# Kernel optimization log

Measured on AMD Instinct MI355X. Metric: run time of the kernel, lower is better.

The kernel has to match this reference:

```python
import jax, jax.numpy as jnp
import numpy as np

COUNTS = (16, 8, 8)  # num_scale_layers from __init__


def _conv1d(x, w, b):
    # x: [B, C, L], w: [Cout, Cin, K] (torch Conv1d layout), valid padding, stride 1
    y = jax.lax.conv_general_dilated(
        x, w, window_strides=(1,), padding='VALID',
        dimension_numbers=('NCH', 'OIH', 'NCH'))
    return y + b[None, :, None]


def _maxpool3s2(x):
    # MaxPool1d(kernel=3, stride=2), valid padding
    return jax.lax.reduce_window(x, -jnp.inf, jax.lax.max,
                                 (1, 1, 3), (1, 1, 2), 'VALID')


def setup_inputs() -> dict:
    key = jax.random.key(0)
    ks = jax.random.split(key, 5)
    B, C, N = 64, 512, 64
    scale = 0.03  # ~1/sqrt(C*K), keeps deep relu-conv chain numerically sane
    x = jax.random.normal(ks[0], (B, C, N), jnp.float32)
    w1 = jax.random.normal(ks[1], (C, C, 1), jnp.float32) * scale
    b1 = jax.random.normal(ks[2], (C,), jnp.float32) * scale
    n_k2 = sum(COUNTS) - len(COUNTS)  # 29 kernel-size-2 convs
    w2 = jax.random.normal(ks[3], (n_k2, C, C, 2), jnp.float32) * scale
    b2 = jax.random.normal(ks[4], (n_k2, C), jnp.float32) * scale
    return {"x": x, "w1": w1, "b1": b1, "w2": w2, "b2": b2}


def reference(x, w1, b1, w2, b2):
    B, C, N = x.shape
    x2d = jnp.zeros((B, C, N, N), x.dtype)
    mask = np.eye(N, dtype=bool)  # static: indices are compile-time constants
    k2 = 0
    stride, offset = 1, 0
    for level, count in enumerate(COUNTS):
        for order in range(count):
            if level == 0 and order == 0:
                x = jax.nn.relu(_conv1d(x, w1, b1))
            elif level > 0 and order == 0:
                x = jax.nn.relu(_maxpool3s2(x))
            else:
                x = jax.nn.relu(_conv1d(x, w2[k2], b2[k2]))
                k2 += 1
            i = np.arange(0, N - offset, stride)
            j = np.arange(offset, N, stride)
            # scatter conv output onto strided diagonal of the 2D map
            x2d = x2d.at[:, :, i, j].set(x)
            mask[i, j] = True
            offset += stride
        offset += stride
        stride *= 2
    return x2d, jnp.asarray(mask)
```

## Files before the change

kernel.cpp:

```cpp
#include <hip/hip_runtime.h>

typedef _Float16 f16;
typedef f16 f16x8 __attribute__((ext_vector_type(8)));
typedef f16 f16x4 __attribute__((ext_vector_type(4)));
typedef float f32x4 __attribute__((ext_vector_type(4)));

#define B_ 64
#define C_ 512
#define X2D_ELEMS ((size_t)134217728)
#define CHAIN_PITCH 1104

__device__ __forceinline__ int col_of(int i, int j) {
    const int d = j - i;
    if (d < 0) return -1;
    if (d <= 15) return 64 * d - (d * (d - 1)) / 2 + i;
    if (d >= 17 && d <= 31 && (d & 1) && !(i & 1)) {
        const int v = (d - 17) >> 1;
        return 904 + 24 * v - (v * (v - 1)) / 2 + (i >> 1);
    }
    if (d >= 35 && !((d - 35) & 3) && !(i & 3)) {
        const int v = (d - 35) >> 2;
        return 1068 + 8 * v - (v * (v - 1)) / 2 + (i >> 2);
    }
    return -1;
}

template<int K, int TAPS>
__device__ __forceinline__
void conv_body(const f16* S, const f16* __restrict__ Wl,
               const float* __restrict__ bias, f16* __restrict__ chain,
               int b0, int q, int cb_out, int Lin, int Lout, int G)
{
    const int lane = threadIdx.x & 63, w = threadIdx.x >> 6;
    const int colq = lane & 15, kg = lane >> 4;
    const int cobase = q * 128 + w * 32;
    const f16* wp0 = Wl + (size_t)(cobase + colq) * K + (kg << 3);
    const f16* wp1 = wp0 + (size_t)16 * K;

    int vg[4], vl[4], row0[4]; bool val[4];
    #pragma unroll
    for (int nf = 0; nf < 4; nf++) {
        const int v = nf * 16 + colq;
        vg[nf] = v / Lout; vl[nf] = v - vg[nf] * Lout;
        val[nf] = vg[nf] < G;
        row0[nf] = val[nf] ? vg[nf] * Lin + vl[nf] : 0;
    }

    f32x4 acc0[4] = {}, acc1[4] = {};
    #pragma unroll 4
    for (int k0 = 0; k0 < K; k0 += 32) {
        const f16x8 af0 = *(const f16x8*)(wp0 + k0);
        const f16x8 af1 = *(const f16x8*)(wp1 + k0);
        const int t = (TAPS == 2 && k0 >= 512) ? 1 : 0;
        const int cch = ((k0 & 511) >> 3) + kg;
        #pragma unroll
        for (int nf = 0; nf < 4; nf++) {
            const int r = row0[nf] + t;
            const f16x8 bf = *(const f16x8*)&S[(r << 9) + ((cch ^ (r & 7)) << 3)];
            acc0[nf] = __builtin_amdgcn_mfma_f32_16x16x32_f16(af0, bf, acc0[nf], 0, 0, 0);
            acc1[nf] = __builtin_amdgcn_mfma_f32_16x16x32_f16(af1, bf, acc1[nf], 0, 0, 0);
        }
    }

    const int co0 = cobase + (kg << 2);
    const float4 bb0 = *(const float4*)&bias[co0];
    const float4 bb1 = *(const float4*)&bias[co0 + 16];
    #pragma unroll
    for (int nf = 0; nf < 4; nf++) {
        if (!val[nf]) continue;
        const size_t base = (((size_t)(b0 + vg[nf]) * CHAIN_PITCH + cb_out + vl[nf]) << 9);
        f16x4 h0, h1;
        #pragma unroll
        for (int j = 0; j < 4; j++) {
            h0[j] = (f16)fmaxf(acc0[nf][j] + ((const float*)&bb0)[j], 0.0f);
            h1[j] = (f16)fmaxf(acc1[nf][j] + ((const float*)&bb1)[j], 0.0f);
        }
        *(f16x4*)&chain[base + co0] = h0;
        *(f16x4*)&chain[base + co0 + 16] = h1;
    }
}

template<int POOL>
__global__ __launch_bounds__(256, 2)
void conv_k2(const f16* __restrict__ chainr, int cb_in,
             const f16* __restrict__ Wl, const float* __restrict__ bias,
             f16* __restrict__ chain, int cb_pool, int cb_out,
             int Lin, int Lout, int G)
{
    __shared__ __align__(16) f16 S[64 * 512];
    const int lane = threadIdx.x & 63, wv = threadIdx.x >> 6;
    const int b0 = blockIdx.x * G, q = blockIdx.y;
    const int rows = G * Lin;

    for (int r = wv; r < rows; r += 4) {
        const int g = r / Lin, l = r - g * Lin;
        f16x8 o;
        if (POOL) {
            const f16* src = chainr +
                (((size_t)(b0 + g) * CHAIN_PITCH + cb_in + 2 * l) << 9) + (lane << 3);
            const f16x8 s0 = *(const f16x8*)(src);
            const f16x8 s1 = *(const f16x8*)(src + 512);
            const f16x8 s2 = *(const f16x8*)(src + 1024);
            #pragma unroll
            for (int j = 0; j < 8; j++)
                o[j] = (f16)fmaxf(fmaxf((float)s0[j], (float)s1[j]),
                                  fmaxf((float)s2[j], 0.0f));
            if (q == 0)
                *(f16x8*)&chain[(((size_t)(b0 + g) * CHAIN_PITCH + cb_pool + l) << 9)
                                + (lane << 3)] = o;
        } else {
            o = *(const f16x8*)(chainr +
                (((size_t)(b0 + g) * CHAIN_PITCH + cb_in + l) << 9) + (lane << 3));
        }
        *(f16x8*)&S[(r << 9) + ((lane ^ (r & 7)) << 3)] = o;
    }
    __syncthreads();
    conv_body<1024, 2>(S, Wl, bias, chain, b0, q, cb_out, Lin, Lout, G);
}

__global__ __launch_bounds__(256, 2)
void conv_first(const float* __restrict__ x, const f16* __restrict__ Wf,
                const float* __restrict__ b1, f16* __restrict__ chain)
{
    __shared__ __align__(16) f16 S[64 * 512];
    const int tid = threadIdx.x;
    const int b = blockIdx.x, q = blockIdx.y;
    #pragma unroll 4
    for (int p = 0; p < 32; p++) {
        const int ci = p * 16 + (tid >> 4), l0 = (tid & 15) << 2;
        const float4 v = *(const float4*)&x[(((size_t)b * C_ + ci) << 6) + l0];
        #pragma unroll
        for (int j = 0; j < 4; j++) {
            const int r = l0 + j;
            S[(r << 9) + (((ci >> 3) ^ (r & 7)) << 3) + (ci & 7)] =
                (f16)((const float*)&v)[j];
        }
    }
    __syncthreads();
    conv_body<512, 1>(S, Wf, b1, chain, b, q, 0, 64, 64, 1);
}

__global__ void prep_all(const float* __restrict__ w1, const float* __restrict__ w2,
                         f16* __restrict__ Wf, float* __restrict__ maskp)
{
    const unsigned idx = blockIdx.x * 256 + threadIdx.x;
    if (idx < 4096u)
        maskp[idx] = (col_of(idx >> 6, idx & 63) >= 0) ? 1.0f : 0.0f;
    if (idx < 262144u) {
        Wf[idx] = (f16)w1[idx];
    } else if (idx < 30u * 262144u) {
        const unsigned r = idx - 262144u;
        const int k2 = r >> 18;
        const unsigned rem = r & 262143u;
        const int co = rem >> 9, ci = rem & 511;
        const float2 v = *(const float2*)&w2[((((size_t)k2 << 9) + co) << 10) + (ci << 1)];
        f16* base = Wf + 262144 + ((size_t)k2 << 19) + ((size_t)co << 10);
        base[ci] = (f16)v.x;
        base[512 + ci] = (f16)v.y;
    }
}

__global__ __launch_bounds__(256)
void assemble3(const f16* __restrict__ chain, float* __restrict__ x2d)
{
    __shared__ __align__(16) f16 J[64 * 512];
    const int tid = threadIdx.x, lane = tid & 63, wv = tid >> 6;
    const int i = blockIdx.x, b = blockIdx.y;

    for (int j = wv; j < 64; j += 4) {
        const int col = col_of(i, j);
        f16x8 v = {0, 0, 0, 0, 0, 0, 0, 0};
        if (col >= 0)
            v = *(const f16x8*)(chain + (((size_t)b * CHAIN_PITCH + col) << 9) + (lane << 3));
        *(f16x8*)&J[(j << 9) + ((lane ^ (j & 7)) << 3)] = v;
    }
    __syncthreads();

    const int jq = tid & 15, c0 = tid >> 4;
    float* dst0 = x2d + (((size_t)b * C_) << 12) + (i << 6) + (jq << 2);
    for (int ct = 0; ct < 32; ct++) {
        const int c = c0 + (ct << 4);
        const int cj = c >> 3;
        float4 o;
        #pragma unroll
        for (int jj = 0; jj < 4; jj++) {
            const int j = (jq << 2) + jj;
            ((float*)&o)[jj] = (float)J[(j << 9) + ((cj ^ (j & 7)) << 3) + (c & 7)];
        }
        *(float4*)(dst0 + ((size_t)c << 12)) = o;
    }
}

extern "C" void kernel_launch(void* const* d_in, const int* in_sizes, int n_in,
                              void* d_out, int out_size, void* d_ws, size_t ws_size,
                              hipStream_t stream)
{
    const float* x  = (const float*)d_in[0];
    const float* w1 = (const float*)d_in[1];
    const float* b1 = (const float*)d_in[2];
    const float* w2 = (const float*)d_in[3];
    const float* b2 = (const float*)d_in[4];
    float* x2d   = (float*)d_out;
    float* maskp = x2d + X2D_ELEMS;

    f16* chain = (f16*)d_ws;
    f16* Wf    = (f16*)x2d;

    prep_all<<<(30 * 262144) / 256, 256, 0, stream>>>(w1, w2, Wf, maskp);

    conv_first<<<dim3(64, 4), 256, 0, stream>>>(x, Wf, b1, chain);

    int L = 64, cb = 64, prev = 0, k2 = 0;
    for (int i = 0; i < 15; i++) {
        conv_k2<0><<<dim3(64, 4), 256, 0, stream>>>(
            chain, prev, Wf + 262144 + (size_t)k2 * 524288, b2 + (size_t)k2 * C_,
            chain, 0, cb, L, L - 1, 1);
        k2++; prev = cb; cb += L - 1; L--;
    }

    conv_k2<1><<<dim3(32, 4), 256, 0, stream>>>(
        chain, prev, Wf + 262144 + (size_t)k2 * 524288, b2 + (size_t)k2 * C_,
        chain, 904, 928, 24, 23, 2);
    k2++; L = 23; prev = 928; cb = 951;
    for (int i = 0; i < 6; i++) {
        conv_k2<0><<<dim3(32, 4), 256, 0, stream>>>(
            chain, prev, Wf + 262144 + (size_t)k2 * 524288, b2 + (size_t)k2 * C_,
            chain, 0, cb, L, L - 1, 2);
        k2++; prev = cb; cb += L - 1; L--;
    }

    conv_k2<1><<<dim3(8, 4), 256, 0, stream>>>(
        chain, prev, Wf + 262144 + (size_t)k2 * 524288, b2 + (size_t)k2 * C_,
        chain, 1068, 1076, 8, 7, 8);
    k2++; L = 7; prev = 1076; cb = 1083;
    for (int i = 0; i < 6; i++) {
        conv_k2<0><<<dim3(8, 4), 256, 0, stream>>>(
            chain, prev, Wf + 262144 + (size_t)k2 * 524288, b2 + (size_t)k2 * C_,
            chain, 0, cb, L, L - 1, 8);
        k2++; prev = cb; cb += L - 1; L--;
    }

    assemble3<<<dim3(64, B_), 256, 0, stream>>>(chain, x2d);
}
```

Before: 759.4 us.

## Retile conv blocks to 64 output channels and overlap assembly with later convs

The conv kernels now tile 64 output channels by 64 positions per block, with a 2x2 wave arrangement, instead of 128 channels by all positions. That raises the block count from 256 to 512 for the early layers. The small-batch conv launches in levels 1 and 2 gain extra blocks that scatter already-finished rows of the 2D output map (rows of later-completed diagonals for batches 4 to 63) while the convs run. This is meant to fill idle CUs during the underoccupied tail layers. The final assembly kernel then only handles the remaining rows, which adds complexity to the indexing and to the ordering dependencies between chain columns.

```diff
diff --git a/kernel.cpp b/kernel.cpp
--- a/kernel.cpp
+++ b/kernel.cpp
@@ -27,76 +27,112 @@
 
 template<int K, int TAPS>
 __device__ __forceinline__
-void conv_body(const f16* S, const f16* __restrict__ Wl,
-               const float* __restrict__ bias, f16* __restrict__ chain,
-               int b0, int q, int cb_out, int Lin, int Lout, int G)
-{
-    const int lane = threadIdx.x & 63, w = threadIdx.x >> 6;
+void conv_body22(const f16* S, const f16* __restrict__ Wl,
+                 const float* __restrict__ bias, f16* __restrict__ chain,
+                 int b0, int m0, int cb_out, int Lin, int Lout, int G)
+{
+    const int lane = threadIdx.x & 63, wv = threadIdx.x >> 6;
+    const int wm = wv >> 1, wn = wv & 1;
     const int colq = lane & 15, kg = lane >> 4;
-    const int cobase = q * 128 + w * 32;
-    const f16* wp0 = Wl + (size_t)(cobase + colq) * K + (kg << 3);
+    const f16* wp0 = Wl + (size_t)(m0 + wm * 32 + colq) * K + (kg << 3);
     const f16* wp1 = wp0 + (size_t)16 * K;
 
-    int vg[4], vl[4], row0[4]; bool val[4];
+    int row0[2], vg[2], vl[2]; bool val[2];
     #pragma unroll
-    for (int nf = 0; nf < 4; nf++) {
-        const int v = nf * 16 + colq;
+    for (int nf = 0; nf < 2; nf++) {
+        const int v = wn * 32 + nf * 16 + colq;
         vg[nf] = v / Lout; vl[nf] = v - vg[nf] * Lout;
         val[nf] = vg[nf] < G;
         row0[nf] = val[nf] ? vg[nf] * Lin + vl[nf] : 0;
     }
 
-    f32x4 acc0[4] = {}, acc1[4] = {};
+    f32x4 acc00 = {}, acc01 = {}, acc10 = {}, acc11 = {};
     #pragma unroll 4
     for (int k0 = 0; k0 < K; k0 += 32) {
         const f16x8 af0 = *(const f16x8*)(wp0 + k0);
         const f16x8 af1 = *(const f16x8*)(wp1 + k0);
         const int t = (TAPS == 2 && k0 >= 512) ? 1 : 0;
         const int cch = ((k0 & 511) >> 3) + kg;
-        #pragma unroll
-        for (int nf = 0; nf < 4; nf++) {
-            const int r = row0[nf] + t;
-            const f16x8 bf = *(const f16x8*)&S[(r << 9) + ((cch ^ (r & 7)) << 3)];
-            acc0[nf] = __builtin_amdgcn_mfma_f32_16x16x32_f16(af0, bf, acc0[nf], 0, 0, 0);
-            acc1[nf] = __builtin_amdgcn_mfma_f32_16x16x32_f16(af1, bf, acc1[nf], 0, 0, 0);
-        }
-    }
-
-    const int co0 = cobase + (kg << 2);
+        const int r0 = row0[0] + t, r1 = row0[1] + t;
+        const f16x8 bf0 = *(const f16x8*)&S[(r0 << 9) + ((cch ^ (r0 & 7)) << 3)];
+        const f16x8 bf1 = *(const f16x8*)&S[(r1 << 9) + ((cch ^ (r1 & 7)) << 3)];
+        acc00 = __builtin_amdgcn_mfma_f32_16x16x32_f16(af0, bf0, acc00, 0, 0, 0);
+        acc10 = __builtin_amdgcn_mfma_f32_16x16x32_f16(af1, bf0, acc10, 0, 0, 0);
+        acc01 = __builtin_amdgcn_mfma_f32_16x16x32_f16(af0, bf1, acc01, 0, 0, 0);
+        acc11 = __builtin_amdgcn_mfma_f32_16x16x32_f16(af1, bf1, acc11, 0, 0, 0);
+    }
+
+    const int co0 = m0 + wm * 32 + (kg << 2);
     const float4 bb0 = *(const float4*)&bias[co0];
     const float4 bb1 = *(const float4*)&bias[co0 + 16];
     #pragma unroll
-    for (int nf = 0; nf < 4; nf++) {
+    for (int nf = 0; nf < 2; nf++) {
         if (!val[nf]) continue;
         const size_t base = (((size_t)(b0 + vg[nf]) * CHAIN_PITCH + cb_out + vl[nf]) << 9);
+        const f32x4 a0 = nf ? acc01 : acc00;
+        const f32x4 a1 = nf ? acc11 : acc10;
         f16x4 h0, h1;
         #pragma unroll
         for (int j = 0; j < 4; j++) {
-            h0[j] = (f16)fmaxf(acc0[nf][j] + ((const float*)&bb0)[j], 0.0f);
-            h1[j] = (f16)fmaxf(acc1[nf][j] + ((const float*)&bb1)[j], 0.0f);
+            h0[j] = (f16)fmaxf(a0[j] + ((const float*)&bb0)[j], 0.0f);
+            h1[j] = (f16)fmaxf(a1[j] + ((const float*)&bb1)[j], 0.0f);
         }
         *(f16x4*)&chain[base + co0] = h0;
         *(f16x4*)&chain[base + co0 + 16] = h1;
     }
 }
 
+__device__ __forceinline__
+void assemble_unit(f16* S, const f16* __restrict__ chain,
+                   float* __restrict__ x2d, int i, int b)
+{
+    const int tid = threadIdx.x, lane = tid & 63, wv = tid >> 6;
+    for (int j = wv; j < 64; j += 4) {
+        const int col = col_of(i, j);
+        f16x8 v = {0, 0, 0, 0, 0, 0, 0, 0};
+        if (col >= 0)
+            v = *(const f16x8*)(chain + (((size_t)b * CHAIN_PITCH + col) << 9) + (lane << 3));
+        *(f16x8*)&S[(j << 9) + ((lane ^ (j & 7)) << 3)] = v;
+    }
+    __syncthreads();
+    const int jq = tid & 15, c0 = tid >> 4;
+    float* dst0 = x2d + (((size_t)b * C_) << 12) + (i << 6) + (jq << 2);
+    for (int ct = 0; ct < 32; ct++) {
+        const int c = c0 + (ct << 4);
+        const int cj = c >> 3;
+        float4 o;
+        #pragma unroll
+        for (int jj = 0; jj < 4; jj++) {
+            const int j = (jq << 2) + jj;
+            ((float*)&o)[jj] = (float)S[(j << 9) + ((cj ^ (j & 7)) << 3) + (c & 7)];
+        }
+        *(float4*)(dst0 + ((size_t)c << 12)) = o;
+    }
+}
+
 template<int POOL>
 __global__ __launch_bounds__(256, 2)
-void conv_k2(const f16* __restrict__ chainr, int cb_in,
-             const f16* __restrict__ Wl, const float* __restrict__ bias,
-             f16* __restrict__ chain, int cb_pool, int cb_out,
-             int Lin, int Lout, int G)
+void conv_k2(int cb_in, const f16* __restrict__ Wl,
+             const float* __restrict__ bias, f16* __restrict__ chain,
+             int cb_pool, int cb_out, int Lin, int Lout, int G, int nbg,
+             float* __restrict__ x2d, int au_base, int au_tot, int row_base)
 {
     __shared__ __align__(16) f16 S[64 * 512];
+    if ((int)blockIdx.y >= nbg) {
+        const int u = au_base + ((int)blockIdx.y - nbg) * 8 + (int)blockIdx.x;
+        if (u >= au_tot) return;
+        assemble_unit(S, chain, x2d, row_base + u / 60, 4 + u % 60);
+        return;
+    }
     const int lane = threadIdx.x & 63, wv = threadIdx.x >> 6;
-    const int b0 = blockIdx.x * G, q = blockIdx.y;
+    const int b0 = blockIdx.y * G, m0 = blockIdx.x * 64;
     const int rows = G * Lin;
 
     for (int r = wv; r < rows; r += 4) {
         const int g = r / Lin, l = r - g * Lin;
         f16x8 o;
         if (POOL) {
-            const f16* src = chainr +
+            const f16* src = chain +
                 (((size_t)(b0 + g) * CHAIN_PITCH + cb_in + 2 * l) << 9) + (lane << 3);
             const f16x8 s0 = *(const f16x8*)(src);
             const f16x8 s1 = *(const f16x8*)(src + 512);
@@ -105,17 +141,17 @@
             for (int j = 0; j < 8; j++)
                 o[j] = (f16)fmaxf(fmaxf((float)s0[j], (float)s1[j]),
                                   fmaxf((float)s2[j], 0.0f));
-            if (q == 0)
+            if (blockIdx.x == 0)
                 *(f16x8*)&chain[(((size_t)(b0 + g) * CHAIN_PITCH + cb_pool + l) << 9)
                                 + (lane << 3)] = o;
         } else {
-            o = *(const f16x8*)(chainr +
+            o = *(const f16x8*)(chain +
                 (((size_t)(b0 + g) * CHAIN_PITCH + cb_in + l) << 9) + (lane << 3));
         }
         *(f16x8*)&S[(r << 9) + ((lane ^ (r & 7)) << 3)] = o;
     }
     __syncthreads();
-    conv_body<1024, 2>(S, Wl, bias, chain, b0, q, cb_out, Lin, Lout, G);
+    conv_body22<1024, 2>(S, Wl, bias, chain, b0, m0, cb_out, Lin, Lout, G);
 }
 
 __global__ __launch_bounds__(256, 2)
@@ -124,7 +160,7 @@
 {
     __shared__ __align__(16) f16 S[64 * 512];
     const int tid = threadIdx.x;
-    const int b = blockIdx.x, q = blockIdx.y;
+    const int b = blockIdx.y, m0 = blockIdx.x * 64;
     #pragma unroll 4
     for (int p = 0; p < 32; p++) {
         const int ci = p * 16 + (tid >> 4), l0 = (tid & 15) << 2;
@@ -137,7 +173,7 @@
         }
     }
     __syncthreads();
-    conv_body<512, 1>(S, Wf, b1, chain, b, q, 0, 64, 64, 1);
+    conv_body22<512, 1>(S, Wf, b1, chain, b, m0, 0, 64, 64, 1);
 }
 
 __global__ void prep_all(const float* __restrict__ w1, const float* __restrict__ w2,
@@ -161,34 +197,14 @@
 }
 
 __global__ __launch_bounds__(256)
-void assemble3(const f16* __restrict__ chain, float* __restrict__ x2d)
-{
-    __shared__ __align__(16) f16 J[64 * 512];
-    const int tid = threadIdx.x, lane = tid & 63, wv = tid >> 6;
-    const int i = blockIdx.x, b = blockIdx.y;
-
-    for (int j = wv; j < 64; j += 4) {
-        const int col = col_of(i, j);
-        f16x8 v = {0, 0, 0, 0, 0, 0, 0, 0};
-        if (col >= 0)
-            v = *(const f16x8*)(chain + (((size_t)b * CHAIN_PITCH + col) << 9) + (lane << 3));
-        *(f16x8*)&J[(j << 9) + ((lane ^ (j & 7)) << 3)] = v;
-    }
-    __syncthreads();
-
-    const int jq = tid & 15, c0 = tid >> 4;
-    float* dst0 = x2d + (((size_t)b * C_) << 12) + (i << 6) + (jq << 2);
-    for (int ct = 0; ct < 32; ct++) {
-        const int c = c0 + (ct << 4);
-        const int cj = c >> 3;
-        float4 o;
-        #pragma unroll
-        for (int jj = 0; jj < 4; jj++) {
-            const int j = (jq << 2) + jj;
-            ((float*)&o)[jj] = (float)J[(j << 9) + ((cj ^ (j & 7)) << 3) + (c & 7)];
-        }
-        *(float4*)(dst0 + ((size_t)c << 12)) = o;
-    }
+void assemble_fin(const f16* __restrict__ chain, float* __restrict__ x2d)
+{
+    __shared__ __align__(16) f16 S[64 * 512];
+    const int u = blockIdx.x;
+    int i, b;
+    if (u < 2112) { i = u >> 6; b = u & 63; }
+    else { const int v = u - 2112; i = 33 + (v >> 2); b = v & 3; }
+    assemble_unit(S, chain, x2d, i, b);
 }
 
 extern "C" void kernel_launch(void* const* d_in, const int* in_sizes, int n_in,
@@ -208,37 +224,37 @@
 
     prep_all<<<(30 * 262144) / 256, 256, 0, stream>>>(w1, w2, Wf, maskp);
 
-    conv_first<<<dim3(64, 4), 256, 0, stream>>>(x, Wf, b1, chain);
+    conv_first<<<dim3(8, 64), 256, 0, stream>>>(x, Wf, b1, chain);
 
     int L = 64, cb = 64, prev = 0, k2 = 0;
     for (int i = 0; i < 15; i++) {
-        conv_k2<0><<<dim3(64, 4), 256, 0, stream>>>(
-            chain, prev, Wf + 262144 + (size_t)k2 * 524288, b2 + (size_t)k2 * C_,
-            chain, 0, cb, L, L - 1, 1);
+        conv_k2<0><<<dim3(8, 64), 256, 0, stream>>>(
+            prev, Wf + 262144 + (size_t)k2 * 524288, b2 + (size_t)k2 * C_,
+            chain, 0, cb, L, L - 1, 1, 64, x2d, 0, 0, 0);
         k2++; prev = cb; cb += L - 1; L--;
     }
 
-    conv_k2<1><<<dim3(32, 4), 256, 0, stream>>>(
-        chain, prev, Wf + 262144 + (size_t)k2 * 524288, b2 + (size_t)k2 * C_,
-        chain, 904, 928, 24, 23, 2);
+    conv_k2<1><<<dim3(8, 52), 256, 0, stream>>>(
+        prev, Wf + 262144 + (size_t)k2 * 524288, b2 + (size_t)k2 * C_,
+        chain, 904, 928, 24, 23, 2, 32, x2d, 0, 1020, 47);
     k2++; L = 23; prev = 928; cb = 951;
     for (int i = 0; i < 6; i++) {
-        conv_k2<0><<<dim3(32, 4), 256, 0, stream>>>(
-            chain, prev, Wf + 262144 + (size_t)k2 * 524288, b2 + (size_t)k2 * C_,
-            chain, 0, cb, L, L - 1, 2);
+        conv_k2<0><<<dim3(8, 52), 256, 0, stream>>>(
+            prev, Wf + 262144 + (size_t)k2 * 524288, b2 + (size_t)k2 * C_,
+            chain, 0, cb, L, L - 1, 2, 32, x2d, (i + 1) * 160, 1020, 47);
         k2++; prev = cb; cb += L - 1; L--;
     }
 
-    conv_k2<1><<<dim3(8, 4), 256, 0, stream>>>(
-        chain, prev, Wf + 262144 + (size_t)k2 * 524288, b2 + (size_t)k2 * C_,
-        chain, 1068, 1076, 8, 7, 8);
+    conv_k2<1><<<dim3(8, 24), 256, 0, stream>>>(
+        prev, Wf + 262144 + (size_t)k2 * 524288, b2 + (size_t)k2 * C_,
+        chain, 1068, 1076, 8, 7, 8, 8, x2d, 0, 840, 33);
     k2++; L = 7; prev = 1076; cb = 1083;
     for (int i = 0; i < 6; i++) {
-        conv_k2<0><<<dim3(8, 4), 256, 0, stream>>>(
-            chain, prev, Wf + 262144 + (size_t)k2 * 524288, b2 + (size_t)k2 * C_,
-            chain, 0, cb, L, L - 1, 8);
+        conv_k2<0><<<dim3(8, 24), 256, 0, stream>>>(
+            prev, Wf + 262144 + (size_t)k2 * 524288, b2 + (size_t)k2 * C_,
+            chain, 0, cb, L, L - 1, 8, 8, x2d, (i + 1) * 128, 840, 33);
         k2++; prev = cb; cb += L - 1; L--;
     }
 
-    assemble3<<<dim3(64, B_), 256, 0, stream>>>(chain, x2d);
-}
+    assemble_fin<<<2236, 256, 0, stream>>>(chain, x2d);
+}
```

Result: no change. 750.3 us (-1.2%).
